# Kernel tuning notes

Hardware: AMD Instinct MI355X
Metric: run time of the kernel (lower is better)

Reference implementation:

```python
import jax, jax.numpy as jnp
import numpy as np

N_HEAD = 16


def setup_inputs() -> dict:
    key = jax.random.key(0)
    k1, k2, k3 = jax.random.split(key, 3)
    B, T, C = 4, 1024, 1024
    x = jax.random.normal(k1, (B, T, C), dtype=jnp.float32)
    w_attn = jax.random.normal(k2, (3 * C, C), dtype=jnp.float32) * 0.02
    w_proj = jax.random.normal(k3, (C, C), dtype=jnp.float32) * 0.02
    return {"x": x, "w_attn": w_attn, "w_proj": w_proj}


def reference(x, w_attn, w_proj):
    B, T, C = x.shape
    H = N_HEAD
    hs = C // H
    scale = 1.0 / np.sqrt(hs).astype(np.float32)

    qkv = x @ w_attn.T                         # [B, T, 3C]
    q, k, v = jnp.split(qkv, 3, axis=-1)
    q = q.reshape(B, T, H, hs).transpose(0, 2, 1, 3)   # [B, H, T, hs]
    k = k.reshape(B, T, H, hs).transpose(0, 2, 1, 3)
    v = v.reshape(B, T, H, hs).transpose(0, 2, 1, 3)

    scores = jnp.einsum('bhqd,bhkd->bhqk', q, k) * scale   # [B, H, T, T]
    causal = jnp.tril(jnp.ones((T, T), dtype=bool))
    scores = jnp.where(causal, scores, -jnp.inf)

    att = jax.nn.sigmoid(scores)                # sigmoid attention, not softmax
    # Bernoulli straight-through sampling (value = sample, grad flows via att)
    samp_key = jax.random.fold_in(jax.random.key(0), 42)
    samples = jax.random.bernoulli(samp_key, att).astype(att.dtype)
    att = att + jax.lax.stop_gradient(samples - att)

    y = jnp.einsum('bhqk,bhkd->bhqd', att, v)   # [B, H, T, hs]
    att_sum = att.sum(axis=-1)                  # [B, H, T]
    att_var = (att * (1.0 - att)).sum(axis=-1)  # [B, H, T]

    y = y.transpose(0, 2, 1, 3).reshape(B, T, C)
    y = y @ w_proj.T
    return (y, att_sum, att_var)
```

## Files before the change

kernel.cpp:

```cpp
#include <hip/hip_runtime.h>
#include <stdint.h>


#define T_SEQ 1024
#define QKV_LD 3072

typedef __attribute__((ext_vector_type(8))) short bf16x8;
typedef __attribute__((ext_vector_type(4))) float f32x4;
typedef __attribute__((ext_vector_type(4))) unsigned int u32x4;

#define ROTL(x, d) __builtin_amdgcn_alignbit((x), (x), 32 - (d))

__device__ __forceinline__ void threefry2x32(uint32_t k0, uint32_t k1,
                                             uint32_t x0, uint32_t x1,
                                             uint32_t &o0, uint32_t &o1) {
  uint32_t ks2 = k0 ^ k1 ^ 0x1BD11BDAu;
#define TF_R4(a, b, c, d)                                                      \
  x0 += x1; x1 = ROTL(x1, a); x1 ^= x0;                                        \
  x0 += x1; x1 = ROTL(x1, b); x1 ^= x0;                                        \
  x0 += x1; x1 = ROTL(x1, c); x1 ^= x0;                                        \
  x0 += x1; x1 = ROTL(x1, d); x1 ^= x0;
  x0 += k0; x1 += k1;
  TF_R4(13, 15, 26, 6)
  x0 += k1; x1 += ks2 + 1u;
  TF_R4(17, 29, 16, 24)
  x0 += ks2; x1 += k0 + 2u;
  TF_R4(13, 15, 26, 6)
  x0 += k0; x1 += k1 + 3u;
  TF_R4(17, 29, 16, 24)
  x0 += k1; x1 += ks2 + 4u;
  TF_R4(13, 15, 26, 6)
  x0 += ks2; x1 += k0 + 5u;
  o0 = x0; o1 = x1;
#undef TF_R4
}

__device__ __forceinline__ unsigned short f2bf(float f) {
  uint32_t u = __float_as_uint(f);
  u += 0x7FFFu + ((u >> 16) & 1u);
  return (unsigned short)(u >> 16);
}

__global__ __launch_bounds__(256) void cvt_bf16(const float4* __restrict__ in,
                                                uint2* __restrict__ out) {
  int i = blockIdx.x * 256 + threadIdx.x;
  float4 v = in[i];
  uint2 o;
  o.x = (uint32_t)f2bf(v.x) | ((uint32_t)f2bf(v.y) << 16);
  o.y = (uint32_t)f2bf(v.z) | ((uint32_t)f2bf(v.w) << 16);
  out[i] = o;
}

template <int OUT_BF16>
__global__ __launch_bounds__(256) void gemm_bf16(const unsigned short* __restrict__ A,
                                                 const unsigned short* __restrict__ B,
                                                 void* __restrict__ Cout,
                                                 int M, int N, int K) {
  __shared__ uint32_t As4[128 * 16];
  __shared__ uint32_t Bs4[128 * 16];

  const int t = threadIdx.x;
  const int lane = t & 63, w = t >> 6;
  const int g = lane >> 4, lr = lane & 15;
  const int rw = w >> 1, cw = w & 1;
  const int bm = blockIdx.x * 128, bn = blockIdx.y * 128;

  const int sr = t >> 1, sp = t & 1;
  const unsigned short* Asrc = A + (size_t)(bm + sr) * K + 16 * sp;
  const unsigned short* Bsrc = B + (size_t)(bn + sr) * K + 16 * sp;
  const int swz = (sr & 3) << 2;
  const int w0 = (8 * sp) ^ swz;
  const int w1 = (8 * sp + 4) ^ swz;

  f32x4 acc[4][4];
#pragma unroll
  for (int i = 0; i < 4; ++i)
#pragma unroll
    for (int j = 0; j < 4; ++j) acc[i][j] = (f32x4){0.f, 0.f, 0.f, 0.f};

  const int wcA = (4 * g) ^ ((lr & 3) << 2);

  u32x4 a0 = *(const u32x4*)(Asrc);
  u32x4 a1 = *(const u32x4*)(Asrc + 8);
  u32x4 b0 = *(const u32x4*)(Bsrc);
  u32x4 b1 = *(const u32x4*)(Bsrc + 8);

  for (int k0 = 0; k0 < K; k0 += 32) {
    __syncthreads();
    *(u32x4*)&As4[sr * 16 + w0] = a0;
    *(u32x4*)&As4[sr * 16 + w1] = a1;
    *(u32x4*)&Bs4[sr * 16 + w0] = b0;
    *(u32x4*)&Bs4[sr * 16 + w1] = b1;
    __syncthreads();

    const int kn = (k0 + 32 < K) ? k0 + 32 : 0;
    a0 = *(const u32x4*)(Asrc + kn);
    a1 = *(const u32x4*)(Asrc + kn + 8);
    b0 = *(const u32x4*)(Bsrc + kn);
    b1 = *(const u32x4*)(Bsrc + kn + 8);

    bf16x8 af[4], bfr[4];
#pragma unroll
    for (int i = 0; i < 4; ++i)
      af[i] = *(const bf16x8*)&As4[(64 * rw + 16 * i + lr) * 16 + wcA];
#pragma unroll
    for (int j = 0; j < 4; ++j)
      bfr[j] = *(const bf16x8*)&Bs4[(64 * cw + 16 * j + lr) * 16 + wcA];
#pragma unroll
    for (int i = 0; i < 4; ++i)
#pragma unroll
      for (int j = 0; j < 4; ++j)
        acc[i][j] = __builtin_amdgcn_mfma_f32_16x16x32_bf16(af[i], bfr[j], acc[i][j], 0, 0, 0);
  }

#pragma unroll
  for (int i = 0; i < 4; ++i)
#pragma unroll
    for (int j = 0; j < 4; ++j)
#pragma unroll
      for (int r = 0; r < 4; ++r) {
        const size_t row = bm + 64 * rw + 16 * i + 4 * g + r;
        const size_t col = bn + 64 * cw + 16 * j + lr;
        if (OUT_BF16)
          ((unsigned short*)Cout)[row * N + col] = f2bf(acc[i][j][r]);
        else
          ((float*)Cout)[row * N + col] = acc[i][j][r];
      }
}

__global__ __launch_bounds__(256) void attn_mfma(const unsigned short* __restrict__ qkv,
                                                 unsigned short* __restrict__ yatt,
                                                 float* __restrict__ att_sum) {
  __shared__ uint32_t Qs4[64 * 32];
  __shared__ uint32_t Ks4[64 * 32];
  __shared__ uint32_t Vt4[64 * 32];
  __shared__ float St[64 * 68];

  const int t = threadIdx.x;
  const int lane = t & 63, w = t >> 6;
  const int g = lane >> 4, lr = lane & 15;
  const int bh = blockIdx.x;
  const int b = bh >> 4, h = bh & 15;
  const int qt = 15 - (int)blockIdx.y;
  const int qt64 = qt * 64;

  uint32_t dk0, dk1;
  threefry2x32(0u, 0u, 0u, 42u, dk0, dk1);

  const unsigned short* qbase = qkv + (size_t)(b * T_SEQ + qt64) * QKV_LD + h * 64;
  {
    const int r = t >> 2, s4 = t & 3;
    const unsigned short* src = qbase + (size_t)r * QKV_LD + 8 * s4;
    u32x4 v0 = *(const u32x4*)(src);
    u32x4 v1 = *(const u32x4*)(src + 32);
    const int sw = (r & 7) << 2;
    *(u32x4*)&Qs4[r * 32 + ((4 * s4) ^ sw)] = v0;
    *(u32x4*)&Qs4[r * 32 + ((4 * s4 + 16) ^ sw)] = v1;
  }
  __syncthreads();

  const int swzr = (lr & 7) << 2;
  bf16x8 aq0, aq1;
  {
    const uint32_t* qrow = &Qs4[(16 * w + lr) * 32];
    aq0 = *(const bf16x8*)&qrow[(4 * g) ^ swzr];
    aq1 = *(const bf16x8*)&qrow[(4 * g + 16) ^ swzr];
  }

  f32x4 yacc[4];
#pragma unroll
  for (int c = 0; c < 4; ++c) yacc[c] = (f32x4){0.f, 0.f, 0.f, 0.f};
  float rs[4] = {0.f, 0.f, 0.f, 0.f};

  for (int kt = 0; kt <= qt; ++kt) {
    __syncthreads();
    const unsigned short* kb = qkv + (size_t)(b * T_SEQ + kt * 64) * QKV_LD + 1024 + h * 64;
    {
      const int r = t >> 2, s4 = t & 3;
      const unsigned short* src = kb + (size_t)r * QKV_LD + 8 * s4;
      u32x4 v0 = *(const u32x4*)(src);
      u32x4 v1 = *(const u32x4*)(src + 32);
      const int sw = (r & 7) << 2;
      *(u32x4*)&Ks4[r * 32 + ((4 * s4) ^ sw)] = v0;
      *(u32x4*)&Ks4[r * 32 + ((4 * s4 + 16) ^ sw)] = v1;
    }
    {
      const int k2 = 2 * (t & 31), d0 = 8 * (t >> 5);
      const unsigned short* vsrc =
          qkv + (size_t)(b * T_SEQ + kt * 64 + k2) * QKV_LD + 2048 + h * 64 + d0;
      union { u32x4 v; unsigned short us[8]; } va, vb;
      va.v = *(const u32x4*)(vsrc);
      vb.v = *(const u32x4*)(vsrc + QKV_LD);
#pragma unroll
      for (int j = 0; j < 8; ++j) {
        uint32_t pw = (uint32_t)va.us[j] | ((uint32_t)vb.us[j] << 16);
        Vt4[(d0 + j) * 32 + ((t & 31) ^ ((j & 7) << 2))] = pw;
      }
    }
    __syncthreads();

    const int kt64 = kt * 64;
#pragma unroll
    for (int c = 0; c < 4; ++c) {
      const uint32_t* krow = &Ks4[(16 * c + lr) * 32];
      bf16x8 bk0 = *(const bf16x8*)&krow[(4 * g) ^ swzr];
      bf16x8 bk1 = *(const bf16x8*)&krow[(4 * g + 16) ^ swzr];
      f32x4 s = __builtin_amdgcn_mfma_f32_16x16x32_bf16(aq0, bk0, (f32x4){0.f, 0.f, 0.f, 0.f}, 0, 0, 0);
      s = __builtin_amdgcn_mfma_f32_16x16x32_bf16(aq1, bk1, s, 0, 0, 0);

      const int kg = kt64 + 16 * c + lr;
#pragma unroll
      for (int r = 0; r < 4; ++r) {
        const int qg = qt64 + 16 * w + 4 * g + r;
        float samp = 0.f;
        if (kg <= qg) {
          float e = __expf(-0.125f * s[r]);
          uint32_t idx = ((uint32_t)bh << 20) | ((uint32_t)qg << 10) | (uint32_t)kg;
          uint32_t r0, r1;
          threefry2x32(dk0, dk1, 0u, idx, r0, r1);
          float u = __uint_as_float(0x3F800000u | ((r0 ^ r1) >> 9)) - 1.0f;
          samp = (u * (1.0f + e) < 1.0f) ? 1.0f : 0.0f;
        }
        rs[r] += samp;
        St[(16 * w + 4 * g + r) * 68 + 16 * c + lr] = samp;
      }
    }

#pragma unroll
    for (int ks = 0; ks < 2; ++ks) {
      const float* prow = &St[(16 * w + lr) * 68 + 8 * g + 32 * ks];
      f32x4 p0 = *(const f32x4*)(prow);
      f32x4 p1 = *(const f32x4*)(prow + 4);
      union { uint32_t u[4]; bf16x8 v; } pa;
      pa.u[0] = (__float_as_uint(p0.y) & 0xFFFF0000u) | (__float_as_uint(p0.x) >> 16);
      pa.u[1] = (__float_as_uint(p0.w) & 0xFFFF0000u) | (__float_as_uint(p0.z) >> 16);
      pa.u[2] = (__float_as_uint(p1.y) & 0xFFFF0000u) | (__float_as_uint(p1.x) >> 16);
      pa.u[3] = (__float_as_uint(p1.w) & 0xFFFF0000u) | (__float_as_uint(p1.z) >> 16);
#pragma unroll
      for (int c = 0; c < 4; ++c) {
        bf16x8 vb = *(const bf16x8*)&Vt4[(16 * c + lr) * 32 + ((4 * g + 16 * ks) ^ swzr)];
        yacc[c] = __builtin_amdgcn_mfma_f32_16x16x32_bf16(pa.v, vb, yacc[c], 0, 0, 0);
      }
    }
  }

  const size_t yb = (size_t)(b * T_SEQ + qt64 + 16 * w) * 1024 + h * 64;
#pragma unroll
  for (int c = 0; c < 4; ++c)
#pragma unroll
    for (int r = 0; r < 4; ++r)
      yatt[yb + (size_t)(4 * g + r) * 1024 + 16 * c + lr] = f2bf(yacc[c][r]);

#pragma unroll
  for (int r = 0; r < 4; ++r) {
    rs[r] += __shfl_xor(rs[r], 1);
    rs[r] += __shfl_xor(rs[r], 2);
    rs[r] += __shfl_xor(rs[r], 4);
    rs[r] += __shfl_xor(rs[r], 8);
  }
  if (lr == 0) {
#pragma unroll
    for (int r = 0; r < 4; ++r)
      att_sum[(size_t)bh * T_SEQ + qt64 + 16 * w + 4 * g + r] = rs[r];
  }
}

__global__ void zero_f4(float4* __restrict__ p) {
  p[(size_t)blockIdx.x * 256 + threadIdx.x] = make_float4(0.f, 0.f, 0.f, 0.f);
}

extern "C" void kernel_launch(void* const* d_in, const int* in_sizes, int n_in,
                              void* d_out, int out_size, void* d_ws, size_t ws_size,
                              hipStream_t stream) {
  (void)in_sizes; (void)n_in; (void)out_size; (void)ws_size;
  const float* x      = (const float*)d_in[0];
  const float* w_attn = (const float*)d_in[1];
  const float* w_proj = (const float*)d_in[2];

  float* y_out      = (float*)d_out;
  float* attsum_out = y_out + (size_t)4 * 1024 * 1024;
  float* attvar_out = attsum_out + (size_t)4 * 16 * 1024;

  unsigned short* ws  = (unsigned short*)d_ws;
  unsigned short* x_bf   = ws;
  unsigned short* wa_bf  = x_bf + (size_t)4 * 1024 * 1024;
  unsigned short* wp_bf  = wa_bf + (size_t)3 * 1024 * 1024;
  unsigned short* qkv_bf = wp_bf + (size_t)1024 * 1024;
  unsigned short* yatt_bf = qkv_bf + (size_t)4096 * 3072;

  dim3 blk(256);
  cvt_bf16<<<dim3(4096), blk, 0, stream>>>((const float4*)x, (uint2*)x_bf);
  cvt_bf16<<<dim3(3072), blk, 0, stream>>>((const float4*)w_attn, (uint2*)wa_bf);
  cvt_bf16<<<dim3(1024), blk, 0, stream>>>((const float4*)w_proj, (uint2*)wp_bf);

  gemm_bf16<1><<<dim3(32, 24), blk, 0, stream>>>(x_bf, wa_bf, (void*)qkv_bf, 4096, 3072, 1024);
  attn_mfma<<<dim3(64, 16), blk, 0, stream>>>(qkv_bf, yatt_bf, attsum_out);
  gemm_bf16<0><<<dim3(32, 8), blk, 0, stream>>>(yatt_bf, wp_bf, (void*)y_out, 4096, 1024, 1024);
  zero_f4<<<dim3(64), blk, 0, stream>>>((float4*)attvar_out);
}
```

Before: 169.3 us.

## Merge conversions, use direct global-to-LDS GEMM loads, pair causal tiles in attention

The three fp32-to-bf16 conversion launches are merged into one kernel, and zeroing att_var moves into the attention kernel, which removes separate launches. The GEMM now loads tiles with global_load_lds straight into shared memory, dropping the register prefetch and the swizzle. Attention blocks each handle a pair of query tiles (qt and 15-qt) to balance causal work, and the bh order is remapped. Q and score storage share one swizzled LDS buffer. The unswizzled GEMM LDS reads risk bank conflicts, and the GEMM loses its overlap of the next load with compute.

```diff
diff --git a/kernel.cpp b/kernel.cpp
--- a/kernel.cpp
+++ b/kernel.cpp
@@ -8,6 +8,9 @@
 typedef __attribute__((ext_vector_type(8))) short bf16x8;
 typedef __attribute__((ext_vector_type(4))) float f32x4;
 typedef __attribute__((ext_vector_type(4))) unsigned int u32x4;
+
+typedef __attribute__((address_space(3))) uint32_t lds_u32;
+typedef __attribute__((address_space(1))) const uint32_t g_u32;
 
 #define ROTL(x, d) __builtin_amdgcn_alignbit((x), (x), 32 - (d))
 
@@ -41,10 +44,21 @@
   return (unsigned short)(u >> 16);
 }
 
-__global__ __launch_bounds__(256) void cvt_bf16(const float4* __restrict__ in,
-                                                uint2* __restrict__ out) {
-  int i = blockIdx.x * 256 + threadIdx.x;
-  float4 v = in[i];
+#define N_X4  1048576
+#define N_WA4 786432
+#define N_WP4 262144
+
+__global__ __launch_bounds__(256) void cvt3_bf16(const float4* __restrict__ x,
+                                                 const float4* __restrict__ wa,
+                                                 const float4* __restrict__ wp,
+                                                 uint2* __restrict__ out) {
+  size_t i = (size_t)blockIdx.x * 256 + threadIdx.x;
+  const float4* src;
+  size_t off;
+  if (i < N_X4) { src = x; off = i; }
+  else if (i < N_X4 + N_WA4) { src = wa; off = i - N_X4; }
+  else { src = wp; off = i - (N_X4 + N_WA4); }
+  float4 v = src[off];
   uint2 o;
   o.x = (uint32_t)f2bf(v.x) | ((uint32_t)f2bf(v.y) << 16);
   o.y = (uint32_t)f2bf(v.z) | ((uint32_t)f2bf(v.w) << 16);
@@ -56,8 +70,8 @@
                                                  const unsigned short* __restrict__ B,
                                                  void* __restrict__ Cout,
                                                  int M, int N, int K) {
-  __shared__ uint32_t As4[128 * 16];
-  __shared__ uint32_t Bs4[128 * 16];
+  __shared__ unsigned short As[128 * 32];
+  __shared__ unsigned short Bs[128 * 32];
 
   const int t = threadIdx.x;
   const int lane = t & 63, w = t >> 6;
@@ -65,47 +79,34 @@
   const int rw = w >> 1, cw = w & 1;
   const int bm = blockIdx.x * 128, bn = blockIdx.y * 128;
 
-  const int sr = t >> 1, sp = t & 1;
-  const unsigned short* Asrc = A + (size_t)(bm + sr) * K + 16 * sp;
-  const unsigned short* Bsrc = B + (size_t)(bn + sr) * K + 16 * sp;
-  const int swz = (sr & 3) << 2;
-  const int w0 = (8 * sp) ^ swz;
-  const int w1 = (8 * sp + 4) ^ swz;
+  const unsigned short* Ag = A + (size_t)(bm + 32 * w + (lane >> 2)) * K + 8 * (lane & 3);
+  const unsigned short* Bg = B + (size_t)(bn + 32 * w + (lane >> 2)) * K + 8 * (lane & 3);
+  lds_u32* Al0 = (lds_u32*)&As[(32 * w) * 32];
+  lds_u32* Al1 = (lds_u32*)&As[(32 * w + 16) * 32];
+  lds_u32* Bl0 = (lds_u32*)&Bs[(32 * w) * 32];
+  lds_u32* Bl1 = (lds_u32*)&Bs[(32 * w + 16) * 32];
 
   f32x4 acc[4][4];
 #pragma unroll
   for (int i = 0; i < 4; ++i)
 #pragma unroll
     for (int j = 0; j < 4; ++j) acc[i][j] = (f32x4){0.f, 0.f, 0.f, 0.f};
-
-  const int wcA = (4 * g) ^ ((lr & 3) << 2);
-
-  u32x4 a0 = *(const u32x4*)(Asrc);
-  u32x4 a1 = *(const u32x4*)(Asrc + 8);
-  u32x4 b0 = *(const u32x4*)(Bsrc);
-  u32x4 b1 = *(const u32x4*)(Bsrc + 8);
 
   for (int k0 = 0; k0 < K; k0 += 32) {
     __syncthreads();
-    *(u32x4*)&As4[sr * 16 + w0] = a0;
-    *(u32x4*)&As4[sr * 16 + w1] = a1;
-    *(u32x4*)&Bs4[sr * 16 + w0] = b0;
-    *(u32x4*)&Bs4[sr * 16 + w1] = b1;
+    __builtin_amdgcn_global_load_lds((g_u32*)(const void*)(Ag + k0), Al0, 16, 0, 0);
+    __builtin_amdgcn_global_load_lds((g_u32*)(const void*)(Ag + k0 + (size_t)16 * K), Al1, 16, 0, 0);
+    __builtin_amdgcn_global_load_lds((g_u32*)(const void*)(Bg + k0), Bl0, 16, 0, 0);
+    __builtin_amdgcn_global_load_lds((g_u32*)(const void*)(Bg + k0 + (size_t)16 * K), Bl1, 16, 0, 0);
     __syncthreads();
 
-    const int kn = (k0 + 32 < K) ? k0 + 32 : 0;
-    a0 = *(const u32x4*)(Asrc + kn);
-    a1 = *(const u32x4*)(Asrc + kn + 8);
-    b0 = *(const u32x4*)(Bsrc + kn);
-    b1 = *(const u32x4*)(Bsrc + kn + 8);
-
     bf16x8 af[4], bfr[4];
 #pragma unroll
     for (int i = 0; i < 4; ++i)
-      af[i] = *(const bf16x8*)&As4[(64 * rw + 16 * i + lr) * 16 + wcA];
+      af[i] = *(const bf16x8*)&As[(64 * rw + 16 * i + lr) * 32 + 8 * g];
 #pragma unroll
     for (int j = 0; j < 4; ++j)
-      bfr[j] = *(const bf16x8*)&Bs4[(64 * cw + 16 * j + lr) * 16 + wcA];
+      bfr[j] = *(const bf16x8*)&Bs[(64 * cw + 16 * j + lr) * 32 + 8 * g];
 #pragma unroll
     for (int i = 0; i < 4; ++i)
 #pragma unroll
@@ -130,143 +131,149 @@
 
 __global__ __launch_bounds__(256) void attn_mfma(const unsigned short* __restrict__ qkv,
                                                  unsigned short* __restrict__ yatt,
-                                                 float* __restrict__ att_sum) {
-  __shared__ uint32_t Qs4[64 * 32];
+                                                 float* __restrict__ att_sum,
+                                                 float* __restrict__ att_var) {
   __shared__ uint32_t Ks4[64 * 32];
   __shared__ uint32_t Vt4[64 * 32];
-  __shared__ float St[64 * 68];
+  __shared__ uint32_t QSt[64 * 72];
 
   const int t = threadIdx.x;
   const int lane = t & 63, w = t >> 6;
   const int g = lane >> 4, lr = lane & 15;
-  const int bh = blockIdx.x;
+  const int gid = blockIdx.x;
+  const int bh = (gid & 7) * 8 + ((gid >> 3) & 7);
+  const int pr = gid >> 6;
   const int b = bh >> 4, h = bh & 15;
-  const int qt = 15 - (int)blockIdx.y;
-  const int qt64 = qt * 64;
 
   uint32_t dk0, dk1;
   threefry2x32(0u, 0u, 0u, 42u, dk0, dk1);
 
-  const unsigned short* qbase = qkv + (size_t)(b * T_SEQ + qt64) * QKV_LD + h * 64;
-  {
-    const int r = t >> 2, s4 = t & 3;
-    const unsigned short* src = qbase + (size_t)r * QKV_LD + 8 * s4;
-    u32x4 v0 = *(const u32x4*)(src);
-    u32x4 v1 = *(const u32x4*)(src + 32);
-    const int sw = (r & 7) << 2;
-    *(u32x4*)&Qs4[r * 32 + ((4 * s4) ^ sw)] = v0;
-    *(u32x4*)&Qs4[r * 32 + ((4 * s4 + 16) ^ sw)] = v1;
-  }
-  __syncthreads();
-
   const int swzr = (lr & 7) << 2;
-  bf16x8 aq0, aq1;
-  {
-    const uint32_t* qrow = &Qs4[(16 * w + lr) * 32];
-    aq0 = *(const bf16x8*)&qrow[(4 * g) ^ swzr];
-    aq1 = *(const bf16x8*)&qrow[(4 * g + 16) ^ swzr];
-  }
-
-  f32x4 yacc[4];
-#pragma unroll
-  for (int c = 0; c < 4; ++c) yacc[c] = (f32x4){0.f, 0.f, 0.f, 0.f};
-  float rs[4] = {0.f, 0.f, 0.f, 0.f};
-
-  for (int kt = 0; kt <= qt; ++kt) {
+
+#pragma unroll 1
+  for (int half = 0; half < 2; ++half) {
+    const int qt = half == 0 ? (15 - pr) : pr;
+    const int qt64 = qt * 64;
+
     __syncthreads();
-    const unsigned short* kb = qkv + (size_t)(b * T_SEQ + kt * 64) * QKV_LD + 1024 + h * 64;
     {
+      const unsigned short* qbase = qkv + (size_t)(b * T_SEQ + qt64) * QKV_LD + h * 64;
       const int r = t >> 2, s4 = t & 3;
-      const unsigned short* src = kb + (size_t)r * QKV_LD + 8 * s4;
+      const unsigned short* src = qbase + (size_t)r * QKV_LD + 8 * s4;
       u32x4 v0 = *(const u32x4*)(src);
       u32x4 v1 = *(const u32x4*)(src + 32);
       const int sw = (r & 7) << 2;
-      *(u32x4*)&Ks4[r * 32 + ((4 * s4) ^ sw)] = v0;
-      *(u32x4*)&Ks4[r * 32 + ((4 * s4 + 16) ^ sw)] = v1;
-    }
+      *(u32x4*)&QSt[r * 72 + ((4 * s4) ^ sw)] = v0;
+      *(u32x4*)&QSt[r * 72 + ((4 * s4 + 16) ^ sw)] = v1;
+    }
+    __syncthreads();
+
+    bf16x8 aq0, aq1;
     {
-      const int k2 = 2 * (t & 31), d0 = 8 * (t >> 5);
-      const unsigned short* vsrc =
-          qkv + (size_t)(b * T_SEQ + kt * 64 + k2) * QKV_LD + 2048 + h * 64 + d0;
-      union { u32x4 v; unsigned short us[8]; } va, vb;
-      va.v = *(const u32x4*)(vsrc);
-      vb.v = *(const u32x4*)(vsrc + QKV_LD);
-#pragma unroll
-      for (int j = 0; j < 8; ++j) {
-        uint32_t pw = (uint32_t)va.us[j] | ((uint32_t)vb.us[j] << 16);
-        Vt4[(d0 + j) * 32 + ((t & 31) ^ ((j & 7) << 2))] = pw;
-      }
-    }
-    __syncthreads();
-
-    const int kt64 = kt * 64;
-#pragma unroll
-    for (int c = 0; c < 4; ++c) {
-      const uint32_t* krow = &Ks4[(16 * c + lr) * 32];
-      bf16x8 bk0 = *(const bf16x8*)&krow[(4 * g) ^ swzr];
-      bf16x8 bk1 = *(const bf16x8*)&krow[(4 * g + 16) ^ swzr];
-      f32x4 s = __builtin_amdgcn_mfma_f32_16x16x32_bf16(aq0, bk0, (f32x4){0.f, 0.f, 0.f, 0.f}, 0, 0, 0);
-      s = __builtin_amdgcn_mfma_f32_16x16x32_bf16(aq1, bk1, s, 0, 0, 0);
-
-      const int kg = kt64 + 16 * c + lr;
-#pragma unroll
-      for (int r = 0; r < 4; ++r) {
-        const int qg = qt64 + 16 * w + 4 * g + r;
-        float samp = 0.f;
-        if (kg <= qg) {
-          float e = __expf(-0.125f * s[r]);
-          uint32_t idx = ((uint32_t)bh << 20) | ((uint32_t)qg << 10) | (uint32_t)kg;
-          uint32_t r0, r1;
-          threefry2x32(dk0, dk1, 0u, idx, r0, r1);
-          float u = __uint_as_float(0x3F800000u | ((r0 ^ r1) >> 9)) - 1.0f;
-          samp = (u * (1.0f + e) < 1.0f) ? 1.0f : 0.0f;
+      const uint32_t* qrow = &QSt[(16 * w + lr) * 72];
+      aq0 = *(const bf16x8*)&qrow[(4 * g) ^ swzr];
+      aq1 = *(const bf16x8*)&qrow[(4 * g + 16) ^ swzr];
+    }
+
+    f32x4 yacc[4];
+#pragma unroll
+    for (int c = 0; c < 4; ++c) yacc[c] = (f32x4){0.f, 0.f, 0.f, 0.f};
+    float rs[4] = {0.f, 0.f, 0.f, 0.f};
+
+    for (int kt = 0; kt <= qt; ++kt) {
+      __syncthreads();
+      const unsigned short* kb = qkv + (size_t)(b * T_SEQ + kt * 64) * QKV_LD + 1024 + h * 64;
+      {
+        const int r = t >> 2, s4 = t & 3;
+        const unsigned short* src = kb + (size_t)r * QKV_LD + 8 * s4;
+        u32x4 v0 = *(const u32x4*)(src);
+        u32x4 v1 = *(const u32x4*)(src + 32);
+        const int sw = (r & 7) << 2;
+        *(u32x4*)&Ks4[r * 32 + ((4 * s4) ^ sw)] = v0;
+        *(u32x4*)&Ks4[r * 32 + ((4 * s4 + 16) ^ sw)] = v1;
+      }
+      {
+        const int k2 = 2 * (t & 31), d0 = 8 * (t >> 5);
+        const unsigned short* vsrc =
+            qkv + (size_t)(b * T_SEQ + kt * 64 + k2) * QKV_LD + 2048 + h * 64 + d0;
+        union { u32x4 v; unsigned short us[8]; } va, vb;
+        va.v = *(const u32x4*)(vsrc);
+        vb.v = *(const u32x4*)(vsrc + QKV_LD);
+#pragma unroll
+        for (int j = 0; j < 8; ++j) {
+          uint32_t pw = (uint32_t)va.us[j] | ((uint32_t)vb.us[j] << 16);
+          Vt4[(d0 + j) * 32 + ((t & 31) ^ ((j & 7) << 2))] = pw;
         }
-        rs[r] += samp;
-        St[(16 * w + 4 * g + r) * 68 + 16 * c + lr] = samp;
-      }
-    }
-
-#pragma unroll
-    for (int ks = 0; ks < 2; ++ks) {
-      const float* prow = &St[(16 * w + lr) * 68 + 8 * g + 32 * ks];
-      f32x4 p0 = *(const f32x4*)(prow);
-      f32x4 p1 = *(const f32x4*)(prow + 4);
-      union { uint32_t u[4]; bf16x8 v; } pa;
-      pa.u[0] = (__float_as_uint(p0.y) & 0xFFFF0000u) | (__float_as_uint(p0.x) >> 16);
-      pa.u[1] = (__float_as_uint(p0.w) & 0xFFFF0000u) | (__float_as_uint(p0.z) >> 16);
-      pa.u[2] = (__float_as_uint(p1.y) & 0xFFFF0000u) | (__float_as_uint(p1.x) >> 16);
-      pa.u[3] = (__float_as_uint(p1.w) & 0xFFFF0000u) | (__float_as_uint(p1.z) >> 16);
+      }
+      __syncthreads();
+
+      const int kt64 = kt * 64;
 #pragma unroll
       for (int c = 0; c < 4; ++c) {
-        bf16x8 vb = *(const bf16x8*)&Vt4[(16 * c + lr) * 32 + ((4 * g + 16 * ks) ^ swzr)];
-        yacc[c] = __builtin_amdgcn_mfma_f32_16x16x32_bf16(pa.v, vb, yacc[c], 0, 0, 0);
-      }
-    }
+        const uint32_t* krow = &Ks4[(16 * c + lr) * 32];
+        bf16x8 bk0 = *(const bf16x8*)&krow[(4 * g) ^ swzr];
+        bf16x8 bk1 = *(const bf16x8*)&krow[(4 * g + 16) ^ swzr];
+        f32x4 s = __builtin_amdgcn_mfma_f32_16x16x32_bf16(aq0, bk0, (f32x4){0.f, 0.f, 0.f, 0.f}, 0, 0, 0);
+        s = __builtin_amdgcn_mfma_f32_16x16x32_bf16(aq1, bk1, s, 0, 0, 0);
+
+        const int kg = kt64 + 16 * c + lr;
+#pragma unroll
+        for (int r = 0; r < 4; ++r) {
+          const int qg = qt64 + 16 * w + 4 * g + r;
+          float samp = 0.f;
+          if (kg <= qg) {
+            float e = __expf(-0.125f * s[r]);
+            uint32_t idx = ((uint32_t)bh << 20) | ((uint32_t)qg << 10) | (uint32_t)kg;
+            uint32_t r0, r1;
+            threefry2x32(dk0, dk1, 0u, idx, r0, r1);
+            float u = __uint_as_float(0x3F800000u | ((r0 ^ r1) >> 9)) - 1.0f;
+            samp = (fmaf(u, e, u) < 1.0f) ? 1.0f : 0.0f;
+          }
+          rs[r] += samp;
+          const int row = 16 * w + 4 * g + r;
+          ((float*)QSt)[row * 72 + ((16 * c + lr) ^ ((row & 7) << 2))] = samp;
+        }
+      }
+
+#pragma unroll
+      for (int ks = 0; ks < 2; ++ks) {
+        const float* srow = (const float*)&QSt[(16 * w + lr) * 72];
+        f32x4 p0 = *(const f32x4*)&srow[(8 * g + 32 * ks) ^ swzr];
+        f32x4 p1 = *(const f32x4*)&srow[(8 * g + 32 * ks + 4) ^ swzr];
+        union { uint32_t u[4]; bf16x8 v; } pa;
+        pa.u[0] = (__float_as_uint(p0.y) & 0xFFFF0000u) | (__float_as_uint(p0.x) >> 16);
+        pa.u[1] = (__float_as_uint(p0.w) & 0xFFFF0000u) | (__float_as_uint(p0.z) >> 16);
+        pa.u[2] = (__float_as_uint(p1.y) & 0xFFFF0000u) | (__float_as_uint(p1.x) >> 16);
+        pa.u[3] = (__float_as_uint(p1.w) & 0xFFFF0000u) | (__float_as_uint(p1.z) >> 16);
+#pragma unroll
+        for (int c = 0; c < 4; ++c) {
+          bf16x8 vb = *(const bf16x8*)&Vt4[(16 * c + lr) * 32 + ((4 * g + 16 * ks) ^ swzr)];
+          yacc[c] = __builtin_amdgcn_mfma_f32_16x16x32_bf16(pa.v, vb, yacc[c], 0, 0, 0);
+        }
+      }
+    }
+
+    const size_t yb = (size_t)(b * T_SEQ + qt64 + 16 * w) * 1024 + h * 64;
+#pragma unroll
+    for (int c = 0; c < 4; ++c)
+#pragma unroll
+      for (int r = 0; r < 4; ++r)
+        yatt[yb + (size_t)(4 * g + r) * 1024 + 16 * c + lr] = f2bf(yacc[c][r]);
+
+#pragma unroll
+    for (int r = 0; r < 4; ++r) {
+      rs[r] += __shfl_xor(rs[r], 1);
+      rs[r] += __shfl_xor(rs[r], 2);
+      rs[r] += __shfl_xor(rs[r], 4);
+      rs[r] += __shfl_xor(rs[r], 8);
+    }
+    if (lr == 0) {
+#pragma unroll
+      for (int r = 0; r < 4; ++r)
+        att_sum[(size_t)bh * T_SEQ + qt64 + 16 * w + 4 * g + r] = rs[r];
+    }
+    if (t < 64) att_var[(size_t)bh * T_SEQ + qt64 + t] = 0.f;
   }
-
-  const size_t yb = (size_t)(b * T_SEQ + qt64 + 16 * w) * 1024 + h * 64;
-#pragma unroll
-  for (int c = 0; c < 4; ++c)
-#pragma unroll
-    for (int r = 0; r < 4; ++r)
-      yatt[yb + (size_t)(4 * g + r) * 1024 + 16 * c + lr] = f2bf(yacc[c][r]);
-
-#pragma unroll
-  for (int r = 0; r < 4; ++r) {
-    rs[r] += __shfl_xor(rs[r], 1);
-    rs[r] += __shfl_xor(rs[r], 2);
-    rs[r] += __shfl_xor(rs[r], 4);
-    rs[r] += __shfl_xor(rs[r], 8);
-  }
-  if (lr == 0) {
-#pragma unroll
-    for (int r = 0; r < 4; ++r)
-      att_sum[(size_t)bh * T_SEQ + qt64 + 16 * w + 4 * g + r] = rs[r];
-  }
-}
-
-__global__ void zero_f4(float4* __restrict__ p) {
-  p[(size_t)blockIdx.x * 256 + threadIdx.x] = make_float4(0.f, 0.f, 0.f, 0.f);
 }
 
 extern "C" void kernel_launch(void* const* d_in, const int* in_sizes, int n_in,
@@ -281,20 +288,17 @@
   float* attsum_out = y_out + (size_t)4 * 1024 * 1024;
   float* attvar_out = attsum_out + (size_t)4 * 16 * 1024;
 
-  unsigned short* ws  = (unsigned short*)d_ws;
-  unsigned short* x_bf   = ws;
-  unsigned short* wa_bf  = x_bf + (size_t)4 * 1024 * 1024;
-  unsigned short* wp_bf  = wa_bf + (size_t)3 * 1024 * 1024;
-  unsigned short* qkv_bf = wp_bf + (size_t)1024 * 1024;
+  unsigned short* ws_us = (unsigned short*)d_ws;
+  unsigned short* x_bf    = ws_us;
+  unsigned short* wa_bf   = x_bf + (size_t)4 * 1024 * 1024;
+  unsigned short* wp_bf   = wa_bf + (size_t)3 * 1024 * 1024;
+  unsigned short* qkv_bf  = wp_bf + (size_t)1024 * 1024;
   unsigned short* yatt_bf = qkv_bf + (size_t)4096 * 3072;
 
   dim3 blk(256);
-  cvt_bf16<<<dim3(4096), blk, 0, stream>>>((const float4*)x, (uint2*)x_bf);
-  cvt_bf16<<<dim3(3072), blk, 0, stream>>>((const float4*)w_attn, (uint2*)wa_bf);
-  cvt_bf16<<<dim3(1024), blk, 0, stream>>>((const float4*)w_proj, (uint2*)wp_bf);
-
+  cvt3_bf16<<<dim3(8192), blk, 0, stream>>>((const float4*)x, (const float4*)w_attn,
+                                            (const float4*)w_proj, (uint2*)x_bf);
   gemm_bf16<1><<<dim3(32, 24), blk, 0, stream>>>(x_bf, wa_bf, (void*)qkv_bf, 4096, 3072, 1024);
-  attn_mfma<<<dim3(64, 16), blk, 0, stream>>>(qkv_bf, yatt_bf, attsum_out);
+  attn_mfma<<<dim3(512), blk, 0, stream>>>(qkv_bf, yatt_bf, attsum_out, attvar_out);
   gemm_bf16<0><<<dim3(32, 8), blk, 0, stream>>>(yatt_bf, wp_bf, (void*)y_out, 4096, 1024, 1024);
-  zero_f4<<<dim3(64), blk, 0, stream>>>((float4*)attvar_out);
-}
+}
```

Result: no change. 168.3 us (-0.6%).
